# Performance work log

Hardware: AMD Instinct MI355X
Metric: run time of the kernel (lower is better)

Reference implementation:

```python
import jax, jax.numpy as jnp
import numpy as np

N = 8192
E = 262144
NEG = 0.2  # leaky_relu negative slope used throughout


def setup_inputs() -> dict:
    key = jax.random.key(0)
    def rn(i, shape, s=0.05):
        return jax.random.normal(jax.random.fold_in(key, i), shape, jnp.float32) * s
    d = {}
    d["x"] = jax.random.normal(jax.random.fold_in(key, 0), (N, 64), jnp.float32)
    d["edge_index"] = jax.random.randint(jax.random.fold_in(key, 1), (2, E), 0, N, dtype=jnp.int32)
    wshapes = {"w0": (64, 256), "as0": (4, 64), "ad0": (4, 64), "r0": (64, 256),
               "w1": (256, 256), "as1": (4, 64), "ad1": (4, 64), "r1": (256, 256),
               "w2": (256, 64), "as2": (1, 64), "ad2": (1, 64), "r2": (256, 64),
               "p0": (256, 64), "p1": (256, 64),
               "qw": (64, 64), "kw": (64, 64), "vw": (64, 64), "ow": (64, 64),
               "m1w": (64, 64), "m2w": (64, 32), "m3w": (32, 10)}
    for i, (nm, sh) in enumerate(wshapes.items()):
        d[nm] = rn(i + 2, sh)
    for nm, dim in [("g0", 256), ("g1", 256), ("g2", 64)]:
        d[nm] = jnp.ones((dim,), jnp.float32)
    for nm, dim in [("be0", 256), ("be1", 256), ("be2", 64), ("b0", 256), ("b1", 256), ("b2", 64),
                    ("qb", 64), ("kb", 64), ("vb", 64), ("ob", 64), ("m1b", 64), ("m2b", 32), ("m3b", 10)]:
        d[nm] = jnp.zeros((dim,), jnp.float32)
    return d


def _forward(edge_index, x, w0, as0, ad0, b0, g0, be0, r0,
             w1, as1, ad1, b1, g1, be1, r1,
             w2, as2, ad2, b2, g2, be2, r2,
             p0, p1, qw, qb, kw, kb, vw, vb, ow, ob,
             m1w, m1b, m2w, m2b, m3w, m3b):
    n = x.shape[0]
    loops = jnp.arange(n, dtype=edge_index.dtype)
    src = jnp.concatenate([edge_index[0], loops])  # add_self_loops=True
    dst = jnp.concatenate([edge_index[1], loops])

    def gat(h, w, a_s, a_d, b, heads):
        hw = (h @ w).reshape(n, heads, 64)  # [N, H, C]
        # PyG GATConv: e_ij = leaky_relu(att_src . h_j + att_dst . h_i), softmax over in-edges of i
        e = jax.nn.leaky_relu(jnp.sum(hw * a_s, -1)[src] + jnp.sum(hw * a_d, -1)[dst], NEG)  # [Etot, H]
        m = jax.ops.segment_max(e, dst, num_segments=n)
        ex = jnp.exp(e - m[dst])
        den = jax.ops.segment_sum(ex, dst, num_segments=n)
        alpha = ex / (den[dst] + 1e-16)
        out = jax.ops.segment_sum(hw[src] * alpha[:, :, None], dst, num_segments=n)
        return out.reshape(n, heads * 64) + b

    def bn(h, g, bta):  # BatchNorm1d, batch statistics (training-mode math)
        mu = jnp.mean(h, 0)
        var = jnp.var(h, 0)
        return (h - mu) * jax.lax.rsqrt(var + 1e-5) * g + bta

    outs = []
    h = x
    for (w, a_s, a_d, b, g, bt, r, heads) in [
            (w0, as0, ad0, b0, g0, be0, r0, 4),
            (w1, as1, ad1, b1, g1, be1, r1, 4),
            (w2, as2, ad2, b2, g2, be2, r2, 1)]:
        res = h @ r
        h = bn(gat(h, w, a_s, a_d, b, heads), g, bt) + res  # shapes always match here
        h = jax.nn.leaky_relu(h, NEG)
        outs.append(h)

    # JumpingKnowledge 'max' after projecting first two layers to hidden dim
    z = jnp.maximum(jnp.maximum(outs[0] @ p0, outs[1] @ p1), outs[2])  # [N, 64]

    # MultiHeadSelfAttention over all nodes (batch=1 implicit), 2 heads, head_dim=32
    q = (z @ qw + qb).reshape(n, 2, 32)
    k = (z @ kw + kb).reshape(n, 2, 32)
    v = (z @ vw + vb).reshape(n, 2, 32)
    attn = jax.nn.softmax(jnp.einsum('nhd,mhd->hnm', q, k) * (32 ** -0.5), axis=-1)
    z = jnp.einsum('hnm,mhd->nhd', attn, v).reshape(n, 64) @ ow + ob

    # MLP head (no data.batch -> GlobalAttention pool skipped)
    z = jax.nn.leaky_relu(z @ m1w + m1b, NEG)
    z = jax.nn.leaky_relu(z @ m2w + m2b, NEG)
    return z @ m3w + m3b


def reference(x, edge_index, w0, as0, ad0, b0, g0, be0, r0,
              w1, as1, ad1, b1, g1, be1, r1,
              w2, as2, ad2, b2, g2, be2, r2,
              p0, p1, qw, qb, kw, kb, vw, vb, ow, ob,
              m1w, m1b, m2w, m2b, m3w, m3b):
    return _forward(edge_index, x, w0, as0, ad0, b0, g0, be0, r0,
                    w1, as1, ad1, b1, g1, be1, r1,
                    w2, as2, ad2, b2, g2, be2, r2,
                    p0, p1, qw, qb, kw, kb, vw, vb, ow, ob,
                    m1w, m1b, m2w, m2b, m3w, m3b)
```

## Files before the change

kernel.cpp:

```cpp
#include <hip/hip_runtime.h>
#include <hip/hip_bf16.h>


#define NEG 0.2f

__device__ __forceinline__ float leaky(float v) { return v > 0.f ? v : NEG * v; }

__device__ __forceinline__ unsigned bf16u(float x) {
    unsigned u = __float_as_uint(x);
    u += 0x7FFFu + ((u >> 16) & 1u);
    return u >> 16;
}

typedef __attribute__((ext_vector_type(8))) short bf16x8;
typedef __attribute__((ext_vector_type(16))) float f32x16;
typedef __attribute__((ext_vector_type(4))) unsigned uint4v;

__global__ __launch_bounds__(256) void gemm64(
    const float* __restrict__ A, const float* __restrict__ B,
    const float* __restrict__ bias, float* __restrict__ C,
    int M, int N, int K, int act)
{
    __shared__ __align__(16) float As[32][64];
    __shared__ __align__(16) float Bs[32][64];
    const int tx = threadIdx.x & 15, ty = threadIdx.x >> 4;
    const int row0 = blockIdx.y * 64, col0 = blockIdx.x * 64;
    const int ar = threadIdx.x & 63, akq = threadIdx.x >> 6;
    const int bc = threadIdx.x & 15, bk = threadIdx.x >> 4;
    float acc[4][4] = {};
    for (int k0 = 0; k0 < K; k0 += 32) {
        {
            const float* ap = A + (size_t)(row0 + ar) * K + k0 + akq * 8;
            float4 a0 = *(const float4*)ap;
            float4 a1 = *(const float4*)(ap + 4);
            int kb = akq * 8;
            As[kb + 0][ar] = a0.x; As[kb + 1][ar] = a0.y;
            As[kb + 2][ar] = a0.z; As[kb + 3][ar] = a0.w;
            As[kb + 4][ar] = a1.x; As[kb + 5][ar] = a1.y;
            As[kb + 6][ar] = a1.z; As[kb + 7][ar] = a1.w;
        }
#pragma unroll
        for (int j = 0; j < 2; ++j) {
            int kk = bk + j * 16;
            int col = col0 + bc * 4;
            float4 b;
            if (col + 3 < N) {
                b = *(const float4*)&B[(size_t)(k0 + kk) * N + col];
            } else {
                b.x = col < N ? B[(size_t)(k0 + kk) * N + col] : 0.f;
                b.y = col + 1 < N ? B[(size_t)(k0 + kk) * N + col + 1] : 0.f;
                b.z = col + 2 < N ? B[(size_t)(k0 + kk) * N + col + 2] : 0.f;
                b.w = col + 3 < N ? B[(size_t)(k0 + kk) * N + col + 3] : 0.f;
            }
            *(float4*)&Bs[kk][bc * 4] = b;
        }
        __syncthreads();
#pragma unroll
        for (int kk = 0; kk < 32; ++kk) {
            float4 a4 = *(const float4*)&As[kk][ty * 4];
            float4 b4 = *(const float4*)&Bs[kk][tx * 4];
            float a[4] = {a4.x, a4.y, a4.z, a4.w};
            float b[4] = {b4.x, b4.y, b4.z, b4.w};
#pragma unroll
            for (int i = 0; i < 4; ++i)
#pragma unroll
                for (int j = 0; j < 4; ++j) acc[i][j] += a[i] * b[j];
        }
        __syncthreads();
    }
#pragma unroll
    for (int i = 0; i < 4; ++i) {
        int r = row0 + ty * 4 + i;
#pragma unroll
        for (int j = 0; j < 4; ++j) {
            int c = col0 + tx * 4 + j;
            if (c < N) {
                float v = acc[i][j] + (bias ? bias[c] : 0.f);
                if (act) v = leaky(v);
                C[(size_t)r * N + c] = v;
            }
        }
    }
}

__global__ __launch_bounds__(256) void gemm_skinny(
    const float* __restrict__ A, const float* __restrict__ B,
    const float* __restrict__ bias, float* __restrict__ C,
    int M, int N, int K, int act)
{
    __shared__ __align__(16) float As[16][68];
    __shared__ __align__(16) float Bs[64][64];
    const int rr = threadIdx.x >> 4, c4 = threadIdx.x & 15;
    const int row0 = blockIdx.x * 16;
    float acc[4] = {};
    for (int k0 = 0; k0 < K; k0 += 64) {
        {
            int k = k0 + c4 * 4;
            float4 a = {0.f, 0.f, 0.f, 0.f};
            const float* ap = &A[(size_t)(row0 + rr) * K + k];
            if (k + 3 < K) a = *(const float4*)ap;
            else {
                if (k < K) a.x = ap[0];
                if (k + 1 < K) a.y = ap[1];
                if (k + 2 < K) a.z = ap[2];
                if (k + 3 < K) a.w = ap[3];
            }
            *(float4*)&As[rr][c4 * 4] = a;
        }
#pragma unroll
        for (int j = 0; j < 4; ++j) {
            int kk = rr + j * 16;
            int col = c4 * 4;
            float4 b = {0.f, 0.f, 0.f, 0.f};
            if (k0 + kk < K) {
                const float* bp = &B[(size_t)(k0 + kk) * N + col];
                if (col + 3 < N) b = *(const float4*)bp;
                else {
                    if (col < N) b.x = bp[0];
                    if (col + 1 < N) b.y = bp[1];
                    if (col + 2 < N) b.z = bp[2];
                    if (col + 3 < N) b.w = bp[3];
                }
            }
            *(float4*)&Bs[kk][col] = b;
        }
        __syncthreads();
#pragma unroll
        for (int kk = 0; kk < 64; ++kk) {
            float a = As[rr][kk];
            float4 b4 = *(const float4*)&Bs[kk][c4 * 4];
            acc[0] += a * b4.x; acc[1] += a * b4.y;
            acc[2] += a * b4.z; acc[3] += a * b4.w;
        }
        __syncthreads();
    }
    int row = row0 + rr, col = c4 * 4;
#pragma unroll
    for (int j = 0; j < 4; ++j) {
        if (col + j < N) {
            float v = acc[j] + (bias ? bias[col + j] : 0.f);
            if (act) v = leaky(v);
            C[(size_t)row * N + col + j] = v;
        }
    }
}

__global__ void sd_kernel(const float* __restrict__ hw, const float* __restrict__ a_s,
                          const float* __restrict__ a_d, float* __restrict__ sval,
                          float* __restrict__ dval, int Nn, int H)
{
    int i = blockIdx.x * blockDim.x + threadIdx.x;
    if (i >= Nn * H) return;
    int n = i / H, h = i - n * H;
    const float4* row = (const float4*)(hw + (size_t)n * H * 64 + h * 64);
    const float4* as4 = (const float4*)(a_s + h * 64);
    const float4* ad4 = (const float4*)(a_d + h * 64);
    float s = 0.f, d = 0.f;
#pragma unroll
    for (int c = 0; c < 16; ++c) {
        float4 x = row[c], a = as4[c], b = ad4[c];
        s += x.x * a.x + x.y * a.y + x.z * a.z + x.w * a.w;
        d += x.x * b.x + x.y * b.y + x.z * b.z + x.w * b.w;
    }
    sval[i] = s;
    dval[i] = d;
}

__global__ void csr_count(const int* __restrict__ ei, int* __restrict__ cnt, int E) {
    int i = blockIdx.x * 256 + threadIdx.x;
    if (i < E) atomicAdd(&cnt[ei[E + i]], 1);
}

__global__ __launch_bounds__(256) void csr_scan(const int* __restrict__ cnt,
                                                int* __restrict__ rowptr,
                                                int* __restrict__ fill, int Nn)
{
    __shared__ int part[256];
    int t = threadIdx.x;
    int loc[32];
    int s = 0;
#pragma unroll
    for (int j = 0; j < 32; ++j) { loc[j] = s; s += cnt[t * 32 + j]; }
    part[t] = s;
    __syncthreads();
    for (int d = 1; d < 256; d <<= 1) {
        int v = (t >= d) ? part[t - d] : 0;
        __syncthreads();
        part[t] += v;
        __syncthreads();
    }
    int off = (t > 0) ? part[t - 1] : 0;
#pragma unroll
    for (int j = 0; j < 32; ++j) {
        int v = off + loc[j];
        rowptr[t * 32 + j] = v;
        fill[t * 32 + j] = v;
    }
    if (t == 255) rowptr[Nn] = part[255];
}

__global__ void csr_scatter(const int* __restrict__ ei, int* __restrict__ fill,
                            int* __restrict__ srcidx, int E) {
    int i = blockIdx.x * 256 + threadIdx.x;
    if (i < E) {
        int d = ei[E + i];
        int p = atomicAdd(&fill[d], 1);
        srcidx[p] = ei[i];
    }
}

template <int H>
__global__ __launch_bounds__(256) void gat_gather(
    const int* __restrict__ rowptr, const int* __restrict__ srcidx,
    const float* __restrict__ hw, const float* __restrict__ sval,
    const float* __restrict__ dval, float* __restrict__ gout, int Nn)
{
    const int node = blockIdx.x * 4 + (threadIdx.x >> 6);
    const int lane = threadIdx.x & 63;
    const int beg = rowptr[node], end = rowptr[node + 1];
    const int C = H * 64;
    float dv[H], es[H], mh[H], lh[H], inv[H], acc[H];
#pragma unroll
    for (int h = 0; h < H; ++h) {
        dv[h] = dval[node * H + h];
        es[h] = leaky(sval[node * H + h] + dv[h]);
        mh[h] = -1e30f;
        lh[h] = 0.f;
    }
    for (int i = beg + lane; i < end; i += 64) {
        int s = srcidx[i];
#pragma unroll
        for (int h = 0; h < H; ++h)
            mh[h] = fmaxf(mh[h], leaky(sval[s * H + h] + dv[h]));
    }
#pragma unroll
    for (int h = 0; h < H; ++h) {
        float m = mh[h];
        for (int off = 32; off; off >>= 1) m = fmaxf(m, __shfl_xor(m, off));
        mh[h] = fmaxf(m, es[h]);
    }
    for (int i = beg + lane; i < end; i += 64) {
        int s = srcidx[i];
#pragma unroll
        for (int h = 0; h < H; ++h)
            lh[h] += __expf(leaky(sval[s * H + h] + dv[h]) - mh[h]);
    }
#pragma unroll
    for (int h = 0; h < H; ++h) {
        float l = lh[h];
        for (int off = 32; off; off >>= 1) l += __shfl_xor(l, off);
        l += __expf(es[h] - mh[h]);
        inv[h] = 1.f / (l + 1e-16f);
        acc[h] = __expf(es[h] - mh[h]) * inv[h] *
                 hw[(size_t)node * C + h * 64 + lane];
    }
    for (int i = beg; i < end; ++i) {
        int s = srcidx[i];
#pragma unroll
        for (int h = 0; h < H; ++h) {
            float e = leaky(sval[s * H + h] + dv[h]);
            float a = __expf(e - mh[h]) * inv[h];
            acc[h] += a * hw[(size_t)s * C + h * 64 + lane];
        }
    }
#pragma unroll
    for (int h = 0; h < H; ++h)
        gout[(size_t)node * C + h * 64 + lane] = acc[h];
}

__global__ void bn_partial(const float* __restrict__ gout, double* __restrict__ sums,
                           int Nn, int C)
{
    int t = threadIdx.x;
    int c = t % C, sub = t / C, nsub = blockDim.x / C;
    int rbase = blockIdx.x * 32;
    double s = 0.0, sq = 0.0;
    for (int r = rbase + sub; r < rbase + 32; r += nsub) {
        float x = gout[(size_t)r * C + c];
        s += x;
        sq += (double)x * x;
    }
    atomicAdd(&sums[c], s);
    atomicAdd(&sums[C + c], sq);
}

__global__ void bn_finalize(const double* __restrict__ sums, float* __restrict__ mu,
                            float* __restrict__ rstd, int Nn, int C)
{
    int c = threadIdx.x;
    if (c >= C) return;
    double m = sums[c] / Nn;
    double v = sums[C + c] / Nn - m * m;
    mu[c] = (float)m;
    rstd[c] = (float)(1.0 / sqrt(v + 1e-5));
}

__global__ void bn_res_act(const float* __restrict__ gout, const float* __restrict__ res,
                           const float* __restrict__ mu, const float* __restrict__ rstd,
                           const float* __restrict__ g, const float* __restrict__ be,
                           float* __restrict__ out, int total, int C)
{
    int i = blockIdx.x * blockDim.x + threadIdx.x;
    if (i >= total) return;
    int c = i & (C - 1);
    float v = (gout[i] - mu[c]) * rstd[c] * g[c] + be[c] + res[i];
    out[i] = leaky(v);
}

__global__ void jk_max(const float* __restrict__ a, const float* __restrict__ b,
                       const float* __restrict__ c, float* __restrict__ z, int total)
{
    int i = blockIdx.x * blockDim.x + threadIdx.x;
    if (i >= total) return;
    z[i] = fmaxf(fmaxf(a[i], b[i]), c[i]);
}

__global__ void kmax_kernel(const float* __restrict__ kg, unsigned* __restrict__ kmax,
                            int N)
{
    const int c = threadIdx.x & 63, g = threadIdx.x >> 6;
    const int rows = N / (gridDim.x * 4);
    const int r0 = (blockIdx.x * 4 + g) * rows;
    float m = 0.f;
    for (int r = r0; r < r0 + rows; ++r)
        m = fmaxf(m, fabsf(kg[(size_t)r * 64 + c]));
    atomicMax(&kmax[c], __float_as_uint(m));
}

__global__ void qk_prep(const float* __restrict__ zq, const float* __restrict__ zk,
                        const unsigned* __restrict__ kmaxu,
                        __hip_bfloat16* __restrict__ Qb, __hip_bfloat16* __restrict__ Kb,
                        float* __restrict__ bound, int N)
{
    int idx = blockIdx.x * 256 + threadIdx.x;
    if (idx >= 2 * N) return;
    int h = idx / N, row = idx - h * N;
    const float scale = 0.17677669529663687f;
    const float* qp = zq + (size_t)row * 64 + h * 32;
    const float* kp = zk + (size_t)row * 64 + h * 32;
    float b = 0.f;
    unsigned qo[16], ko[16];
#pragma unroll
    for (int i = 0; i < 16; ++i) {
        float q0 = qp[2 * i] * scale, q1 = qp[2 * i + 1] * scale;
        float k0 = kp[2 * i], k1 = kp[2 * i + 1];
        b += fabsf(q0) * __uint_as_float(kmaxu[h * 32 + 2 * i]);
        b += fabsf(q1) * __uint_as_float(kmaxu[h * 32 + 2 * i + 1]);
        qo[i] = bf16u(q0) | (bf16u(q1) << 16);
        ko[i] = bf16u(k0) | (bf16u(k1) << 16);
    }
    uint4* qd = (uint4*)(Qb + (size_t)idx * 32);
    uint4* kd = (uint4*)(Kb + (size_t)idx * 32);
#pragma unroll
    for (int i = 0; i < 4; ++i) {
        qd[i] = make_uint4(qo[4 * i], qo[4 * i + 1], qo[4 * i + 2], qo[4 * i + 3]);
        kd[i] = make_uint4(ko[4 * i], ko[4 * i + 1], ko[4 * i + 2], ko[4 * i + 3]);
    }
    bound[idx] = b;
}

__global__ void v_prep(const float* __restrict__ zv, __hip_bfloat16* __restrict__ Vf,
                       int N)
{
    int idx = blockIdx.x * 256 + threadIdx.x;
    int total = 2 * (N >> 4) * 64;
    if (idx >= total) return;
    int lane = idx & 63;
    int g = (idx >> 6) % (N >> 4);
    int h = (idx >> 6) / (N >> 4);
    int kb = g * 16 + (lane >> 5) * 8;
    int d = (lane & 31) + h * 32;
    unsigned o[4];
#pragma unroll
    for (int i = 0; i < 4; ++i) {
        unsigned u0 = bf16u(zv[(size_t)(kb + 2 * i) * 64 + d]);
        unsigned u1 = bf16u(zv[(size_t)(kb + 2 * i + 1) * 64 + d]);
        o[i] = u0 | (u1 << 16);
    }
    *(uint4*)(Vf + (size_t)idx * 8) = make_uint4(o[0], o[1], o[2], o[3]);
}

__global__ __launch_bounds__(256) void attn_mfma(
    const __hip_bfloat16* __restrict__ Qb, const __hip_bfloat16* __restrict__ Kb,
    const __hip_bfloat16* __restrict__ Vf, const float* __restrict__ bound,
    float* __restrict__ pl, __hip_bfloat16* __restrict__ pacc,
    int N, int nchunk, int chunksz)
{
    const int lane = threadIdx.x & 63;
    const int wid = threadIdx.x >> 6;
    const int hi = lane >> 5, lq = lane & 31;
    const int chunk = blockIdx.x;
    const int qtile = blockIdx.y * 4 + wid;
    const int head = qtile / (N >> 5);
    const int q0 = (qtile % (N >> 5)) * 32;
    const int kbase = chunk * chunksz;

    const size_t qrow = (size_t)head * N + q0 + lq;
    const bf16x8 qf0 = *(const bf16x8*)(Qb + qrow * 32 + hi * 8);
    const bf16x8 qf1 = *(const bf16x8*)(Qb + qrow * 32 + hi * 8 + 16);
    const float bnd = bound[qrow];

    f32x16 oacc;
#pragma unroll
    for (int r = 0; r < 16; ++r) oacc[r] = 0.f;
    float lsum = 0.f;

    for (int kt = kbase; kt < kbase + chunksz; kt += 32) {
        const size_t krow = (size_t)head * N + kt + lq;
        const bf16x8 kf0 = *(const bf16x8*)(Kb + krow * 32 + hi * 8);
        const bf16x8 kf1 = *(const bf16x8*)(Kb + krow * 32 + hi * 8 + 16);
        f32x16 s;
#pragma unroll
        for (int r = 0; r < 16; ++r) s[r] = 0.f;
        s = __builtin_amdgcn_mfma_f32_32x32x16_bf16(kf0, qf0, s, 0, 0, 0);
        s = __builtin_amdgcn_mfma_f32_32x32x16_bf16(kf1, qf1, s, 0, 0, 0);
        const __hip_bfloat16* vfb =
            Vf + (((size_t)head * (N >> 4) + (kt >> 4)) * 64 + lane) * 8;
        const bf16x8 vf0 = *(const bf16x8*)vfb;
        const bf16x8 vf1 = *(const bf16x8*)(vfb + 64 * 8);

        float p[16];
#pragma unroll
        for (int r = 0; r < 16; ++r) p[r] = __expf(s[r] - bnd);
        float ls = 0.f;
#pragma unroll
        for (int r = 0; r < 16; ++r) ls += p[r];
        lsum += ls;

        unsigned wpk[8];
#pragma unroll
        for (int i = 0; i < 8; ++i)
            wpk[i] = bf16u(p[2 * i]) | (bf16u(p[2 * i + 1]) << 16);
        unsigned ws[8];
#pragma unroll
        for (int i = 0; i < 8; ++i) ws[i] = (unsigned)__shfl_xor((int)wpk[i], 32);
        uint4v b1, b2;
        b1[0] = hi ? ws[2] : wpk[0];
        b1[1] = hi ? ws[3] : wpk[1];
        b1[2] = hi ? wpk[2] : ws[0];
        b1[3] = hi ? wpk[3] : ws[1];
        b2[0] = hi ? ws[6] : wpk[4];
        b2[1] = hi ? ws[7] : wpk[5];
        b2[2] = hi ? wpk[6] : ws[4];
        b2[3] = hi ? wpk[7] : ws[5];
        oacc = __builtin_amdgcn_mfma_f32_32x32x16_bf16(
            vf0, __builtin_bit_cast(bf16x8, b1), oacc, 0, 0, 0);
        oacc = __builtin_amdgcn_mfma_f32_32x32x16_bf16(
            vf1, __builtin_bit_cast(bf16x8, b2), oacc, 0, 0, 0);
    }
    lsum += __shfl_xor(lsum, 32);
    const size_t hr = (size_t)head * N + q0 + lq;
    if (hi == 0) pl[hr * nchunk + chunk] = lsum;
    __hip_bfloat16* pb = pacc + (hr * nchunk + chunk) * 32;
#pragma unroll
    for (int rg = 0; rg < 4; ++rg) {
        unsigned lo = bf16u(oacc[rg * 4 + 0]) | (bf16u(oacc[rg * 4 + 1]) << 16);
        unsigned hw2 = bf16u(oacc[rg * 4 + 2]) | (bf16u(oacc[rg * 4 + 3]) << 16);
        *(uint2*)(pb + rg * 8 + hi * 4) = make_uint2(lo, hw2);
    }
}

__global__ void attn_combine(const float* __restrict__ pl,
                             const __hip_bfloat16* __restrict__ pacc,
                             float* __restrict__ og, int N, int nchunk)
{
    int i = blockIdx.x * blockDim.x + threadIdx.x;
    if (i >= 2 * N * 32) return;
    int hr = i >> 5, cc = i & 31;
    float l = 0.f, a = 0.f;
    for (int c = 0; c < nchunk; ++c) {
        l += pl[(size_t)hr * nchunk + c];
        a += __bfloat162float(pacc[((size_t)hr * nchunk + c) * 32 + cc]);
    }
    int head = hr / N, row = hr - head * N;
    og[(size_t)row * 64 + head * 32 + cc] = a / l;
}

extern "C" void kernel_launch(void* const* d_in, const int* in_sizes, int n_in,
                              void* d_out, int out_size, void* d_ws, size_t ws_size,
                              hipStream_t stream)
{
    const float* x = (const float*)d_in[0];
    const int* ei = (const int*)d_in[1];
    const float* w[3]   = {(const float*)d_in[2], (const float*)d_in[6],  (const float*)d_in[10]};
    const float* as_[3] = {(const float*)d_in[3], (const float*)d_in[7],  (const float*)d_in[11]};
    const float* ad_[3] = {(const float*)d_in[4], (const float*)d_in[8],  (const float*)d_in[12]};
    const float* rw[3]  = {(const float*)d_in[5], (const float*)d_in[9],  (const float*)d_in[13]};
    const float* p0 = (const float*)d_in[14];
    const float* p1 = (const float*)d_in[15];
    const float* qw = (const float*)d_in[16];
    const float* kw = (const float*)d_in[17];
    const float* vw = (const float*)d_in[18];
    const float* ow = (const float*)d_in[19];
    const float* m1w = (const float*)d_in[20];
    const float* m2w = (const float*)d_in[21];
    const float* m3w = (const float*)d_in[22];
    const float* g_[3]  = {(const float*)d_in[23], (const float*)d_in[24], (const float*)d_in[25]};
    const float* be_[3] = {(const float*)d_in[26], (const float*)d_in[27], (const float*)d_in[28]};
    const float* qb  = (const float*)d_in[32];
    const float* kb  = (const float*)d_in[33];
    const float* vb  = (const float*)d_in[34];
    const float* ob  = (const float*)d_in[35];
    const float* m1b = (const float*)d_in[36];
    const float* m2b = (const float*)d_in[37];
    const float* m3b = (const float*)d_in[38];

    const int N = in_sizes[0] / 64;
    const int E = in_sizes[1] / 2;

    float* ws = (float*)d_ws;
    size_t off = 0;
    auto alloc = [&](size_t n) {
        float* p = ws + off;
        off += (n + 255) & ~(size_t)255;
        return p;
    };
    float* hw   = alloc((size_t)N * 256);
    float* res  = alloc((size_t)N * 256);
    float* gout = alloc((size_t)N * 256);
    float* h0   = alloc((size_t)N * 256);
    float* h1   = alloc((size_t)N * 256);
    float* h2   = alloc((size_t)N * 64);
    float* sval = alloc((size_t)N * 4);
    float* dval = alloc((size_t)N * 4);
    double* bnsum = (double*)alloc(1024);
    float* mu   = alloc(256);
    float* rstd = alloc(256);
    int* cnt    = (int*)alloc(N);
    int* rowptr = (int*)alloc(N + 256);
    int* fill   = (int*)alloc(N);
    int* srcidx = (int*)alloc(E);
    unsigned* kmaxu = (unsigned*)alloc(64);
    float* zq = hw;
    float* zk = hw + (size_t)N * 64;
    float* zv = hw + 2 * (size_t)N * 64;
    float* ao = hw + 3 * (size_t)N * 64;
    float* z  = gout;
    float* tA = res;
    float* tB = res + (size_t)N * 64;
    float* tC = res + 2 * (size_t)N * 64;
    const int NCHUNK = 8;
    __hip_bfloat16* Qb = (__hip_bfloat16*)h0;
    __hip_bfloat16* Kb = Qb + (size_t)2 * N * 32;
    __hip_bfloat16* Vf = Kb + (size_t)2 * N * 32;
    float* boundArr = (float*)(Vf + (size_t)2 * N * 32);
    __hip_bfloat16* pacc = (__hip_bfloat16*)res;
    float* pl = h2;

    auto gemm = [&](const float* A, const float* B, const float* bias, float* C,
                    int M, int Nc, int K, int act) {
        if (Nc <= 64) {
            gemm_skinny<<<M / 16, 256, 0, stream>>>(A, B, bias, C, M, Nc, K, act);
        } else {
            dim3 grid((Nc + 63) / 64, M / 64);
            gemm64<<<grid, 256, 0, stream>>>(A, B, bias, C, M, Nc, K, act);
        }
    };

    hipMemsetAsync(cnt, 0, (size_t)N * 4, stream);
    csr_count<<<(E + 255) / 256, 256, 0, stream>>>(ei, cnt, E);
    csr_scan<<<1, 256, 0, stream>>>(cnt, rowptr, fill, N);
    csr_scatter<<<(E + 255) / 256, 256, 0, stream>>>(ei, fill, srcidx, E);

    const float* hin = x;
    int Kin = 64;
    float* houts[3] = {h0, h1, h2};
    int heads[3] = {4, 4, 1};

    for (int l = 0; l < 3; ++l) {
        int H = heads[l], C = H * 64;
        gemm(hin, w[l], nullptr, hw, N, C, Kin, 0);
        gemm(hin, rw[l], nullptr, res, N, C, Kin, 0);
        sd_kernel<<<(N * H + 255) / 256, 256, 0, stream>>>(hw, as_[l], ad_[l], sval, dval, N, H);
        if (H == 4)
            gat_gather<4><<<N / 4, 256, 0, stream>>>(rowptr, srcidx, hw, sval, dval, gout, N);
        else
            gat_gather<1><<<N / 4, 256, 0, stream>>>(rowptr, srcidx, hw, sval, dval, gout, N);
        hipMemsetAsync(bnsum, 0, (size_t)2 * C * 8, stream);
        bn_partial<<<N / 32, 256, 0, stream>>>(gout, bnsum, N, C);
        bn_finalize<<<1, 256, 0, stream>>>(bnsum, mu, rstd, N, C);
        bn_res_act<<<((size_t)N * C) / 256, 256, 0, stream>>>(gout, res, mu, rstd, g_[l], be_[l], houts[l], N * C, C);
        hin = houts[l];
        Kin = C;
    }

    gemm(h0, p0, nullptr, tA, N, 64, 256, 0);
    gemm(h1, p1, nullptr, tB, N, 64, 256, 0);
    jk_max<<<((size_t)N * 64) / 256, 256, 0, stream>>>(tA, tB, h2, z, N * 64);

    gemm(z, qw, qb, zq, N, 64, 64, 0);
    gemm(z, kw, kb, zk, N, 64, 64, 0);
    gemm(z, vw, vb, zv, N, 64, 64, 0);
    hipMemsetAsync(kmaxu, 0, 64 * 4, stream);
    kmax_kernel<<<32, 256, 0, stream>>>(zk, kmaxu, N);
    qk_prep<<<(2 * N + 255) / 256, 256, 0, stream>>>(zq, zk, kmaxu, Qb, Kb, boundArr, N);
    v_prep<<<(2 * (N >> 4) * 64 + 255) / 256, 256, 0, stream>>>(zv, Vf, N);
    attn_mfma<<<dim3(NCHUNK, (2 * N / 32) / 4), 256, 0, stream>>>(
        Qb, Kb, Vf, boundArr, pl, pacc, N, NCHUNK, N / NCHUNK);
    attn_combine<<<(2 * N * 32 + 255) / 256, 256, 0, stream>>>(pl, pacc, ao, N, NCHUNK);
    gemm(ao, ow, ob, tA, N, 64, 64, 0);

    gemm(tA, m1w, m1b, tB, N, 64, 64, 1);
    gemm(tB, m2w, m2b, tC, N, 32, 64, 1);
    gemm(tC, m3w, m3b, (float*)d_out, N, 10, 32, 0);
}
```

Before: 470.9 us.

## Replace fp32 SIMT GEMMs with split-bf16 MFMA GEMMs and fused split emission

All dense projections now run through one MFMA kernel that represents fp32 operands as bf16 hi/lo pairs and accumulates three bf16 products, keeping accuracy close to fp32. Weights are split and transposed once per call by a batched kernel. Activation producers (bn_res_act, jk_max, attn_combine, and the GEMM epilogue itself) emit the hi/lo split alongside the fp32 output, so later GEMMs read pre-split inputs. The aim is to move GEMM FLOPs from scalar FMA onto matrix cores. The cost is extra split kernels and stores, and the GEMM reads its operands straight from global memory with no LDS staging. The lo*lo product is dropped, which introduces a small precision loss.

```diff
diff --git a/kernel.cpp b/kernel.cpp
--- a/kernel.cpp
+++ b/kernel.cpp
@@ -16,131 +16,86 @@
 typedef __attribute__((ext_vector_type(16))) float f32x16;
 typedef __attribute__((ext_vector_type(4))) unsigned uint4v;
 
-__global__ __launch_bounds__(256) void gemm64(
-    const float* __restrict__ A, const float* __restrict__ B,
+__device__ __forceinline__ void split1(float v, unsigned& hb, unsigned& lb) {
+    hb = bf16u(v);
+    float hf = __uint_as_float(hb << 16);
+    lb = bf16u(v - hf);
+}
+
+__global__ void split_rows(const float* __restrict__ in,
+                           unsigned short* __restrict__ hi,
+                           unsigned short* __restrict__ lo, int total4)
+{
+    int i = blockIdx.x * 256 + threadIdx.x;
+    if (i >= total4) return;
+    float4 v = ((const float4*)in)[i];
+    float vv[4] = {v.x, v.y, v.z, v.w};
+    ushort4 h, l;
+#pragma unroll
+    for (int j = 0; j < 4; ++j) {
+        unsigned hb, lb;
+        split1(vv[j], hb, lb);
+        (&h.x)[j] = (unsigned short)hb;
+        (&l.x)[j] = (unsigned short)lb;
+    }
+    ((ushort4*)hi)[i] = h;
+    ((ushort4*)lo)[i] = l;
+}
+
+struct WEnt { const float* src; unsigned short* hi; unsigned short* lo; int K; int N; };
+struct WArr { WEnt e[15]; };
+
+__global__ void split_weights(WArr a)
+{
+    WEnt w = a.e[blockIdx.y];
+    int id = blockIdx.x * 256 + threadIdx.x;
+    if (id >= w.K * w.N) return;
+    int k = id / w.N, n = id - k * w.N;
+    unsigned hb, lb;
+    split1(w.src[id], hb, lb);
+    w.hi[(size_t)n * w.K + k] = (unsigned short)hb;
+    w.lo[(size_t)n * w.K + k] = (unsigned short)lb;
+}
+
+__global__ __launch_bounds__(256) void gemm_mfma(
+    const unsigned short* __restrict__ Ahi, const unsigned short* __restrict__ Alo,
+    const unsigned short* __restrict__ Bhi, const unsigned short* __restrict__ Blo,
     const float* __restrict__ bias, float* __restrict__ C,
+    unsigned short* __restrict__ Chi, unsigned short* __restrict__ Clo,
     int M, int N, int K, int act)
 {
-    __shared__ __align__(16) float As[32][64];
-    __shared__ __align__(16) float Bs[32][64];
-    const int tx = threadIdx.x & 15, ty = threadIdx.x >> 4;
-    const int row0 = blockIdx.y * 64, col0 = blockIdx.x * 64;
-    const int ar = threadIdx.x & 63, akq = threadIdx.x >> 6;
-    const int bc = threadIdx.x & 15, bk = threadIdx.x >> 4;
-    float acc[4][4] = {};
-    for (int k0 = 0; k0 < K; k0 += 32) {
-        {
-            const float* ap = A + (size_t)(row0 + ar) * K + k0 + akq * 8;
-            float4 a0 = *(const float4*)ap;
-            float4 a1 = *(const float4*)(ap + 4);
-            int kb = akq * 8;
-            As[kb + 0][ar] = a0.x; As[kb + 1][ar] = a0.y;
-            As[kb + 2][ar] = a0.z; As[kb + 3][ar] = a0.w;
-            As[kb + 4][ar] = a1.x; As[kb + 5][ar] = a1.y;
-            As[kb + 6][ar] = a1.z; As[kb + 7][ar] = a1.w;
-        }
-#pragma unroll
-        for (int j = 0; j < 2; ++j) {
-            int kk = bk + j * 16;
-            int col = col0 + bc * 4;
-            float4 b;
-            if (col + 3 < N) {
-                b = *(const float4*)&B[(size_t)(k0 + kk) * N + col];
-            } else {
-                b.x = col < N ? B[(size_t)(k0 + kk) * N + col] : 0.f;
-                b.y = col + 1 < N ? B[(size_t)(k0 + kk) * N + col + 1] : 0.f;
-                b.z = col + 2 < N ? B[(size_t)(k0 + kk) * N + col + 2] : 0.f;
-                b.w = col + 3 < N ? B[(size_t)(k0 + kk) * N + col + 3] : 0.f;
-            }
-            *(float4*)&Bs[kk][bc * 4] = b;
-        }
-        __syncthreads();
-#pragma unroll
-        for (int kk = 0; kk < 32; ++kk) {
-            float4 a4 = *(const float4*)&As[kk][ty * 4];
-            float4 b4 = *(const float4*)&Bs[kk][tx * 4];
-            float a[4] = {a4.x, a4.y, a4.z, a4.w};
-            float b[4] = {b4.x, b4.y, b4.z, b4.w};
-#pragma unroll
-            for (int i = 0; i < 4; ++i)
-#pragma unroll
-                for (int j = 0; j < 4; ++j) acc[i][j] += a[i] * b[j];
-        }
-        __syncthreads();
-    }
-#pragma unroll
-    for (int i = 0; i < 4; ++i) {
-        int r = row0 + ty * 4 + i;
-#pragma unroll
-        for (int j = 0; j < 4; ++j) {
-            int c = col0 + tx * 4 + j;
-            if (c < N) {
-                float v = acc[i][j] + (bias ? bias[c] : 0.f);
-                if (act) v = leaky(v);
-                C[(size_t)r * N + c] = v;
-            }
-        }
-    }
-}
-
-__global__ __launch_bounds__(256) void gemm_skinny(
-    const float* __restrict__ A, const float* __restrict__ B,
-    const float* __restrict__ bias, float* __restrict__ C,
-    int M, int N, int K, int act)
-{
-    __shared__ __align__(16) float As[16][68];
-    __shared__ __align__(16) float Bs[64][64];
-    const int rr = threadIdx.x >> 4, c4 = threadIdx.x & 15;
-    const int row0 = blockIdx.x * 16;
-    float acc[4] = {};
-    for (int k0 = 0; k0 < K; k0 += 64) {
-        {
-            int k = k0 + c4 * 4;
-            float4 a = {0.f, 0.f, 0.f, 0.f};
-            const float* ap = &A[(size_t)(row0 + rr) * K + k];
-            if (k + 3 < K) a = *(const float4*)ap;
-            else {
-                if (k < K) a.x = ap[0];
-                if (k + 1 < K) a.y = ap[1];
-                if (k + 2 < K) a.z = ap[2];
-                if (k + 3 < K) a.w = ap[3];
-            }
-            *(float4*)&As[rr][c4 * 4] = a;
-        }
-#pragma unroll
-        for (int j = 0; j < 4; ++j) {
-            int kk = rr + j * 16;
-            int col = c4 * 4;
-            float4 b = {0.f, 0.f, 0.f, 0.f};
-            if (k0 + kk < K) {
-                const float* bp = &B[(size_t)(k0 + kk) * N + col];
-                if (col + 3 < N) b = *(const float4*)bp;
-                else {
-                    if (col < N) b.x = bp[0];
-                    if (col + 1 < N) b.y = bp[1];
-                    if (col + 2 < N) b.z = bp[2];
-                    if (col + 3 < N) b.w = bp[3];
-                }
-            }
-            *(float4*)&Bs[kk][col] = b;
-        }
-        __syncthreads();
-#pragma unroll
-        for (int kk = 0; kk < 64; ++kk) {
-            float a = As[rr][kk];
-            float4 b4 = *(const float4*)&Bs[kk][c4 * 4];
-            acc[0] += a * b4.x; acc[1] += a * b4.y;
-            acc[2] += a * b4.z; acc[3] += a * b4.w;
-        }
-        __syncthreads();
-    }
-    int row = row0 + rr, col = c4 * 4;
-#pragma unroll
-    for (int j = 0; j < 4; ++j) {
-        if (col + j < N) {
-            float v = acc[j] + (bias ? bias[col + j] : 0.f);
-            if (act) v = leaky(v);
-            C[(size_t)row * N + col + j] = v;
+    const int lane = threadIdx.x & 63, wid = threadIdx.x >> 6;
+    const int hb4 = lane >> 5, lq = lane & 31;
+    const int row0 = blockIdx.y * 64 + (wid >> 1) * 32;
+    const int col0 = blockIdx.x * 64 + (wid & 1) * 32;
+    const size_t abase = (size_t)(row0 + lq) * K + hb4 * 8;
+    const size_t bbase = (size_t)(col0 + lq) * K + hb4 * 8;
+    f32x16 acc0, acc1;
+#pragma unroll
+    for (int r = 0; r < 16; ++r) { acc0[r] = 0.f; acc1[r] = 0.f; }
+    for (int k0 = 0; k0 < K; k0 += 16) {
+        bf16x8 a_h = *(const bf16x8*)(Ahi + abase + k0);
+        bf16x8 a_l = *(const bf16x8*)(Alo + abase + k0);
+        bf16x8 b_h = *(const bf16x8*)(Bhi + bbase + k0);
+        bf16x8 b_l = *(const bf16x8*)(Blo + bbase + k0);
+        acc0 = __builtin_amdgcn_mfma_f32_32x32x16_bf16(a_h, b_h, acc0, 0, 0, 0);
+        acc1 = __builtin_amdgcn_mfma_f32_32x32x16_bf16(a_l, b_h, acc1, 0, 0, 0);
+        acc1 = __builtin_amdgcn_mfma_f32_32x32x16_bf16(a_h, b_l, acc1, 0, 0, 0);
+    }
+    int col = col0 + lq;
+    if (col >= N) return;
+    float bs = bias ? bias[col] : 0.f;
+#pragma unroll
+    for (int r = 0; r < 16; ++r) {
+        int row = row0 + (r & 3) + 8 * (r >> 2) + 4 * hb4;
+        float v = acc0[r] + acc1[r] + bs;
+        if (act) v = leaky(v);
+        C[(size_t)row * N + col] = v;
+        if (Chi) {
+            unsigned hh, ll;
+            split1(v, hh, ll);
+            Chi[(size_t)row * N + col] = (unsigned short)hh;
+            Clo[(size_t)row * N + col] = (unsigned short)ll;
         }
     }
 }
@@ -298,21 +253,37 @@
 __global__ void bn_res_act(const float* __restrict__ gout, const float* __restrict__ res,
                            const float* __restrict__ mu, const float* __restrict__ rstd,
                            const float* __restrict__ g, const float* __restrict__ be,
-                           float* __restrict__ out, int total, int C)
+                           float* __restrict__ out,
+                           unsigned short* __restrict__ shi,
+                           unsigned short* __restrict__ slo, int total, int C)
 {
     int i = blockIdx.x * blockDim.x + threadIdx.x;
     if (i >= total) return;
     int c = i & (C - 1);
     float v = (gout[i] - mu[c]) * rstd[c] * g[c] + be[c] + res[i];
-    out[i] = leaky(v);
+    v = leaky(v);
+    out[i] = v;
+    if (shi) {
+        unsigned hb, lb;
+        split1(v, hb, lb);
+        shi[i] = (unsigned short)hb;
+        slo[i] = (unsigned short)lb;
+    }
 }
 
 __global__ void jk_max(const float* __restrict__ a, const float* __restrict__ b,
-                       const float* __restrict__ c, float* __restrict__ z, int total)
+                       const float* __restrict__ c, float* __restrict__ z,
+                       unsigned short* __restrict__ shi,
+                       unsigned short* __restrict__ slo, int total)
 {
     int i = blockIdx.x * blockDim.x + threadIdx.x;
     if (i >= total) return;
-    z[i] = fmaxf(fmaxf(a[i], b[i]), c[i]);
+    float v = fmaxf(fmaxf(a[i], b[i]), c[i]);
+    z[i] = v;
+    unsigned hb, lb;
+    split1(v, hb, lb);
+    shi[i] = (unsigned short)hb;
+    slo[i] = (unsigned short)lb;
 }
 
 __global__ void kmax_kernel(const float* __restrict__ kg, unsigned* __restrict__ kmax,
@@ -431,18 +402,18 @@
 #pragma unroll
         for (int i = 0; i < 8; ++i)
             wpk[i] = bf16u(p[2 * i]) | (bf16u(p[2 * i + 1]) << 16);
-        unsigned ws[8];
-#pragma unroll
-        for (int i = 0; i < 8; ++i) ws[i] = (unsigned)__shfl_xor((int)wpk[i], 32);
+        unsigned wsx[8];
+#pragma unroll
+        for (int i = 0; i < 8; ++i) wsx[i] = (unsigned)__shfl_xor((int)wpk[i], 32);
         uint4v b1, b2;
-        b1[0] = hi ? ws[2] : wpk[0];
-        b1[1] = hi ? ws[3] : wpk[1];
-        b1[2] = hi ? wpk[2] : ws[0];
-        b1[3] = hi ? wpk[3] : ws[1];
-        b2[0] = hi ? ws[6] : wpk[4];
-        b2[1] = hi ? ws[7] : wpk[5];
-        b2[2] = hi ? wpk[6] : ws[4];
-        b2[3] = hi ? wpk[7] : ws[5];
+        b1[0] = hi ? wsx[2] : wpk[0];
+        b1[1] = hi ? wsx[3] : wpk[1];
+        b1[2] = hi ? wpk[2] : wsx[0];
+        b1[3] = hi ? wpk[3] : wsx[1];
+        b2[0] = hi ? wsx[6] : wpk[4];
+        b2[1] = hi ? wsx[7] : wpk[5];
+        b2[2] = hi ? wpk[6] : wsx[4];
+        b2[3] = hi ? wpk[7] : wsx[5];
         oacc = __builtin_amdgcn_mfma_f32_32x32x16_bf16(
             vf0, __builtin_bit_cast(bf16x8, b1), oacc, 0, 0, 0);
         oacc = __builtin_amdgcn_mfma_f32_32x32x16_bf16(
@@ -462,7 +433,9 @@
 
 __global__ void attn_combine(const float* __restrict__ pl,
                              const __hip_bfloat16* __restrict__ pacc,
-                             float* __restrict__ og, int N, int nchunk)
+                             float* __restrict__ og,
+                             unsigned short* __restrict__ shi,
+                             unsigned short* __restrict__ slo, int N, int nchunk)
 {
     int i = blockIdx.x * blockDim.x + threadIdx.x;
     if (i >= 2 * N * 32) return;
@@ -473,7 +446,13 @@
         a += __bfloat162float(pacc[((size_t)hr * nchunk + c) * 32 + cc]);
     }
     int head = hr / N, row = hr - head * N;
-    og[(size_t)row * 64 + head * 32 + cc] = a / l;
+    float v = a / l;
+    size_t oi = (size_t)row * 64 + head * 32 + cc;
+    og[oi] = v;
+    unsigned hb, lb;
+    split1(v, hb, lb);
+    shi[oi] = (unsigned short)hb;
+    slo[oi] = (unsigned short)lb;
 }
 
 extern "C" void kernel_launch(void* const* d_in, const int* in_sizes, int n_in,
@@ -531,6 +510,20 @@
     int* fill   = (int*)alloc(N);
     int* srcidx = (int*)alloc(E);
     unsigned* kmaxu = (unsigned*)alloc(64);
+    unsigned short* sAhi = (unsigned short*)alloc((size_t)N * 128);
+    unsigned short* sAlo = (unsigned short*)alloc((size_t)N * 128);
+    unsigned short* sBhi = (unsigned short*)alloc((size_t)N * 32);
+    unsigned short* sBlo = (unsigned short*)alloc((size_t)N * 32);
+    const float* wsrc[15] = {w[0], rw[0], w[1], rw[1], w[2], rw[2], p0, p1,
+                             qw, kw, vw, ow, m1w, m2w, m3w};
+    const int wK[15] = {64, 64, 256, 256, 256, 256, 256, 256, 64, 64, 64, 64, 64, 64, 32};
+    const int wN[15] = {256, 256, 256, 256, 64, 64, 64, 64, 64, 64, 64, 64, 64, 32, 10};
+    unsigned short *whi[15], *wlo[15];
+    for (int i = 0; i < 15; ++i) {
+        int padN = wN[i] < 64 ? 64 : wN[i];
+        whi[i] = (unsigned short*)alloc((size_t)padN * wK[i] / 2);
+        wlo[i] = (unsigned short*)alloc((size_t)padN * wK[i] / 2);
+    }
     float* zq = hw;
     float* zk = hw + (size_t)N * 64;
     float* zv = hw + 2 * (size_t)N * 64;
@@ -547,30 +540,36 @@
     __hip_bfloat16* pacc = (__hip_bfloat16*)res;
     float* pl = h2;
 
-    auto gemm = [&](const float* A, const float* B, const float* bias, float* C,
-                    int M, int Nc, int K, int act) {
-        if (Nc <= 64) {
-            gemm_skinny<<<M / 16, 256, 0, stream>>>(A, B, bias, C, M, Nc, K, act);
-        } else {
-            dim3 grid((Nc + 63) / 64, M / 64);
-            gemm64<<<grid, 256, 0, stream>>>(A, B, bias, C, M, Nc, K, act);
-        }
+    auto gemmM = [&](const unsigned short* Ahi_, const unsigned short* Alo_, int widx,
+                     const float* bias, float* C, unsigned short* Chi,
+                     unsigned short* Clo, int M, int Nc, int K, int act) {
+        dim3 grid((Nc + 63) / 64, M / 64);
+        gemm_mfma<<<grid, 256, 0, stream>>>(Ahi_, Alo_, whi[widx], wlo[widx],
+                                            bias, C, Chi, Clo, M, Nc, K, act);
     };
+
+    {
+        WArr wa;
+        for (int i = 0; i < 15; ++i)
+            wa.e[i] = WEnt{wsrc[i], whi[i], wlo[i], wK[i], wN[i]};
+        split_weights<<<dim3(256, 15), 256, 0, stream>>>(wa);
+    }
 
     hipMemsetAsync(cnt, 0, (size_t)N * 4, stream);
     csr_count<<<(E + 255) / 256, 256, 0, stream>>>(ei, cnt, E);
     csr_scan<<<1, 256, 0, stream>>>(cnt, rowptr, fill, N);
     csr_scatter<<<(E + 255) / 256, 256, 0, stream>>>(ei, fill, srcidx, E);
 
-    const float* hin = x;
-    int Kin = 64;
+    split_rows<<<(N * 64 / 4 + 255) / 256, 256, 0, stream>>>(x, sAhi, sAlo, N * 64 / 4);
+
     float* houts[3] = {h0, h1, h2};
     int heads[3] = {4, 4, 1};
+    int Kin = 64;
 
     for (int l = 0; l < 3; ++l) {
         int H = heads[l], C = H * 64;
-        gemm(hin, w[l], nullptr, hw, N, C, Kin, 0);
-        gemm(hin, rw[l], nullptr, res, N, C, Kin, 0);
+        gemmM(sAhi, sAlo, 2 * l, nullptr, hw, nullptr, nullptr, N, C, Kin, 0);
+        gemmM(sAhi, sAlo, 2 * l + 1, nullptr, res, nullptr, nullptr, N, C, Kin, 0);
         sd_kernel<<<(N * H + 255) / 256, 256, 0, stream>>>(hw, as_[l], ad_[l], sval, dval, N, H);
         if (H == 4)
             gat_gather<4><<<N / 4, 256, 0, stream>>>(rowptr, srcidx, hw, sval, dval, gout, N);
@@ -579,28 +578,32 @@
         hipMemsetAsync(bnsum, 0, (size_t)2 * C * 8, stream);
         bn_partial<<<N / 32, 256, 0, stream>>>(gout, bnsum, N, C);
         bn_finalize<<<1, 256, 0, stream>>>(bnsum, mu, rstd, N, C);
-        bn_res_act<<<((size_t)N * C) / 256, 256, 0, stream>>>(gout, res, mu, rstd, g_[l], be_[l], houts[l], N * C, C);
-        hin = houts[l];
+        bn_res_act<<<((size_t)N * C) / 256, 256, 0, stream>>>(
+            gout, res, mu, rstd, g_[l], be_[l], houts[l],
+            l < 2 ? sAhi : nullptr, l < 2 ? sAlo : nullptr, N * C, C);
         Kin = C;
     }
 
-    gemm(h0, p0, nullptr, tA, N, 64, 256, 0);
-    gemm(h1, p1, nullptr, tB, N, 64, 256, 0);
-    jk_max<<<((size_t)N * 64) / 256, 256, 0, stream>>>(tA, tB, h2, z, N * 64);
-
-    gemm(z, qw, qb, zq, N, 64, 64, 0);
-    gemm(z, kw, kb, zk, N, 64, 64, 0);
-    gemm(z, vw, vb, zv, N, 64, 64, 0);
+    gemmM(sAhi, sAlo, 7, nullptr, tB, nullptr, nullptr, N, 64, 256, 0);
+    split_rows<<<(N * 256 / 4 + 255) / 256, 256, 0, stream>>>(h0, sAhi, sAlo, N * 256 / 4);
+    gemmM(sAhi, sAlo, 6, nullptr, tA, nullptr, nullptr, N, 64, 256, 0);
+    jk_max<<<((size_t)N * 64) / 256, 256, 0, stream>>>(tA, tB, h2, z, sAhi, sAlo, N * 64);
+
+    gemmM(sAhi, sAlo, 8, qb, zq, nullptr, nullptr, N, 64, 64, 0);
+    gemmM(sAhi, sAlo, 9, kb, zk, nullptr, nullptr, N, 64, 64, 0);
+    gemmM(sAhi, sAlo, 10, vb, zv, nullptr, nullptr, N, 64, 64, 0);
+
     hipMemsetAsync(kmaxu, 0, 64 * 4, stream);
     kmax_kernel<<<32, 256, 0, stream>>>(zk, kmaxu, N);
     qk_prep<<<(2 * N + 255) / 256, 256, 0, stream>>>(zq, zk, kmaxu, Qb, Kb, boundArr, N);
     v_prep<<<(2 * (N >> 4) * 64 + 255) / 256, 256, 0, stream>>>(zv, Vf, N);
     attn_mfma<<<dim3(NCHUNK, (2 * N / 32) / 4), 256, 0, stream>>>(
         Qb, Kb, Vf, boundArr, pl, pacc, N, NCHUNK, N / NCHUNK);
-    attn_combine<<<(2 * N * 32 + 255) / 256, 256, 0, stream>>>(pl, pacc, ao, N, NCHUNK);
-    gemm(ao, ow, ob, tA, N, 64, 64, 0);
-
-    gemm(tA, m1w, m1b, tB, N, 64, 64, 1);
-    gemm(tB, m2w, m2b, tC, N, 32, 64, 1);
-    gemm(tC, m3w, m3b, (float*)d_out, N, 10, 32, 0);
-}
+    attn_combine<<<(2 * N * 32 + 255) / 256, 256, 0, stream>>>(
+        pl, pacc, ao, sAhi, sAlo, N, NCHUNK);
+
+    gemmM(sAhi, sAlo, 11, ob, tA, sBhi, sBlo, N, 64, 64, 0);
+    gemmM(sBhi, sBlo, 12, m1b, tB, sAhi, sAlo, N, 64, 64, 1);
+    gemmM(sAhi, sAlo, 13, m2b, tC, sBhi, sBlo, N, 32, 64, 1);
+    gemmM(sBhi, sBlo, 14, m3b, (float*)d_out, nullptr, nullptr, N, 10, 32, 0);
+}
```

After: 458.2 us. 2.7% less time.
